# Kernel tuning notes

Hardware: AMD Instinct MI355X
Metric: run time of the kernel (lower is better)

Reference implementation:

```python
import jax, jax.numpy as jnp
import numpy as np

BATCH = 4096          # batch_size from init
TEMP = 0.1            # temperature
EPS = 1e-8            # torch CosineSimilarity eps
N = 2 * BATCH


def _neg_flat_idx(bs):
    """Static flat indices of the negative entries of the (N,N) sim matrix:
    everything except the main diagonal and the +-bs diagonals (positives)."""
    n = 2 * bs
    mask = np.ones((n, n), dtype=bool)
    np.fill_diagonal(mask, False)
    r = np.arange(bs)
    mask[r, bs + r] = False
    mask[bs + r, r] = False
    return np.nonzero(mask.reshape(-1))[0]


NEG_IDX = jnp.asarray(_neg_flat_idx(BATCH))  # (N*(N-2),)


def setup_inputs() -> dict:
    key = jax.random.key(0)
    k1, k2 = jax.random.split(key)
    msg = jax.random.normal(k1, (N, 512), dtype=jnp.float32)
    img = jax.random.normal(k2, (N, 512), dtype=jnp.float32)
    return {"msg": msg, "img": img}


def reference(msg, img):
    # cosine similarity via normalized GEMM (norms clamped at eps, per torch)
    mn = msg / jnp.maximum(jnp.linalg.norm(msg, axis=1, keepdims=True), EPS)
    im = img / jnp.maximum(jnp.linalg.norm(img, axis=1, keepdims=True), EPS)
    sim = jnp.matmul(mn, im.T) / TEMP                      # (N, N)

    sim_i_j = jnp.diagonal(sim, offset=BATCH)              # (BATCH,)
    sim_j_i = jnp.diagonal(sim, offset=-BATCH)             # (BATCH,)
    positives = jnp.concatenate([sim_i_j, sim_j_i])[:, None]   # (N, 1)
    negatives = sim.reshape(-1)[NEG_IDX].reshape(N, N - 2)     # (N, N-2)

    logits = jnp.concatenate([positives, negatives], axis=1)   # (N, N-1)
    logp = jax.nn.log_softmax(logits, axis=1)
    # labels are all zero; CrossEntropyLoss(reduction='sum') / N
    loss = -jnp.sum(logp[:, 0]) / N
    acc = jnp.mean((jnp.argmax(logits, axis=1) == 0).astype(jnp.float32))
    return loss, acc
```

## Files before the change

### kernel.cpp

```cpp
#include <hip/hip_runtime.h>
#include <hip/hip_bf16.h>


#define NROWS 8192
#define BATCHD 4096
#define DIM 512
#define BM 128
#define BN 256
#define BK 32
#define NT2 (DIM / BK)
#define SHIFT 10.0f

typedef short bf16x8 __attribute__((ext_vector_type(8)));
typedef float f32x4 __attribute__((ext_vector_type(4)));

#define GLDS(g, l)                                                             \
    __builtin_amdgcn_global_load_lds(                                          \
        (const __attribute__((address_space(1))) void*)(g),                    \
        (__attribute__((address_space(3))) void*)(l), 16, 0, 0)

__device__ __forceinline__ unsigned f2u_ord(float f) {
    unsigned u = __float_as_uint(f);
    return (u & 0x80000000u) ? ~u : (u | 0x80000000u);
}
__device__ __forceinline__ float u2f_ord(unsigned e) {
    return (e & 0x80000000u) ? __uint_as_float(e & 0x7fffffffu) : __uint_as_float(~e);
}
__device__ __forceinline__ short f2bf(float f) {
    unsigned u = __float_as_uint(f);
    return (short)((u + 0x7fffu + ((u >> 16) & 1u)) >> 16);
}

__global__ __launch_bounds__(64) void normalize_bf16_both(const float* __restrict__ msg,
                                                          const float* __restrict__ img,
                                                          short* __restrict__ mnb,
                                                          short* __restrict__ imb,
                                                          float* __restrict__ rowsum,
                                                          unsigned* __restrict__ rowmax,
                                                          float* __restrict__ accum) {
    if (blockIdx.x < 128) {
        const int i = blockIdx.x * 64 + threadIdx.x;
        rowsum[i] = 0.f;
        rowmax[i] = 0u;
        if (i < 2) accum[i] = 0.f;
    }
    int row = blockIdx.x;
    const float* in;
    short* out;
    float scale;
    if (row < NROWS) { in = msg; out = mnb; scale = 10.0f; }
    else { row -= NROWS; in = img; out = imb; scale = 1.0f; }
    const int lane = threadIdx.x;
    const float* src = in + (size_t)row * DIM + lane * 8;
    float4 v0 = *(const float4*)(src);
    float4 v1 = *(const float4*)(src + 4);
    float ss = v0.x*v0.x + v0.y*v0.y + v0.z*v0.z + v0.w*v0.w
             + v1.x*v1.x + v1.y*v1.y + v1.z*v1.z + v1.w*v1.w;
    #pragma unroll
    for (int off = 1; off < 64; off <<= 1) ss += __shfl_xor(ss, off);
    const float inv = scale / fmaxf(sqrtf(ss), 1e-8f);
    float vv[8] = {v0.x, v0.y, v0.z, v0.w, v1.x, v1.y, v1.z, v1.w};
    bf16x8 o;
    #pragma unroll
    for (int j = 0; j < 8; ++j) o[j] = f2bf(vv[j] * inv);
    *(bf16x8*)(out + (size_t)row * DIM + lane * 8) = o;
}

__global__ __launch_bounds__(512, 4) void simloss_mfma(const short* __restrict__ A,
                                                       const short* __restrict__ B,
                                                       float* __restrict__ rowsum,
                                                       unsigned* __restrict__ rowmax,
                                                       float* __restrict__ rowpos) {
    __shared__ short As[2][BM * BK];
    __shared__ short Bs[2][BN * BK];

    const int tid = threadIdx.x;
    const int lane = tid & 63;
    const int g = lane >> 4;
    const int r16 = lane & 15;
    const int wid = tid >> 6;
    const int wr = wid >> 2;
    const int wc = wid & 3;

    const int bid = blockIdx.x;
    const int xcd = bid & 7;
    const int l = bid >> 3;
    const int by = xcd * 8 + (l & 7);
    const int bx = l >> 3;
    const int rowBase = by * BM;
    const int colBase = bx * BN;

    const int srow = tid >> 2;
    const int sc = (tid & 3) ^ ((srow >> 1) & 3);
    const short* gA = A + (size_t)(rowBase + srow) * DIM + sc * 8;
    const short* gB = B + (size_t)(colBase + srow) * DIM + sc * 8;

#define STAGE(b, koff)                                      \
    do {                                                    \
        GLDS(gA + (koff), &As[b][tid * 8]);                 \
        GLDS(gB + (koff), &Bs[b][tid * 8]);                 \
        GLDS(gB + 128 * DIM + (koff), &Bs[b][4096 + tid * 8]); \
    } while (0)

    const int swz = (r16 >> 1) & 3;
    const int aBase = (wr * 64 + r16) * BK + ((g ^ swz) * 8);
    const int bBase = (wc * 64 + r16) * BK + ((g ^ swz) * 8);

    f32x4 acc[4][4] = {};

#define VMCNT(n) asm volatile("s_waitcnt vmcnt(" #n ")" ::: "memory")
#define BAR() __builtin_amdgcn_s_barrier()

    STAGE(0, 0);

    for (int t = 0; t < NT2; ++t) {
        const int b = t & 1;
        if (t < NT2 - 1) {
            STAGE(b ^ 1, (t + 1) * BK);
            VMCNT(3);
        } else {
            VMCNT(0);
        }
        BAR();
        bf16x8 af[4], bfr[4];
        #pragma unroll
        for (int m = 0; m < 4; ++m)
            af[m] = *(const bf16x8*)&As[b][aBase + m * 16 * BK];
        #pragma unroll
        for (int n = 0; n < 4; ++n)
            bfr[n] = *(const bf16x8*)&Bs[b][bBase + n * 16 * BK];
        __builtin_amdgcn_s_setprio(1);
        #pragma unroll
        for (int m = 0; m < 4; ++m)
            #pragma unroll
            for (int n = 0; n < 4; ++n)
                acc[m][n] = __builtin_amdgcn_mfma_f32_16x16x32_bf16(
                    af[m], bfr[n], acc[m][n], 0, 0, 0);
        __builtin_amdgcn_s_setprio(0);
        BAR();
    }

    __syncthreads();
    float* ssum = (float*)&As[0][0];
    float* smx = ssum + 512;
    const int baseRowW = rowBase + wr * 64 + g * 4;
    const int baseColW = colBase + wc * 64 + r16;
    #pragma unroll
    for (int m = 0; m < 4; ++m) {
        #pragma unroll
        for (int reg = 0; reg < 4; ++reg) {
            const int i = baseRowW + m * 16 + reg;
            const int partner = i ^ BATCHD;
            float sum = 0.f, mx = -1e30f;
            #pragma unroll
            for (int n = 0; n < 4; ++n) {
                const int j = baseColW + n * 16;
                const float s = acc[m][n][reg];
                const bool isDiag = (j == i);
                const bool isPos = (j == partner);
                float e = __expf(s - SHIFT);
                if (isDiag) e = 0.f;
                sum += e;
                if (!isDiag && !isPos) mx = fmaxf(mx, s);
                if (isPos) rowpos[i] = s;
            }
            #pragma unroll
            for (int off = 1; off < 16; off <<= 1) {
                sum += __shfl_xor(sum, off);
                mx = fmaxf(mx, __shfl_xor(mx, off));
            }
            if (r16 == 0) {
                const int rloc = wr * 64 + m * 16 + g * 4 + reg;
                ssum[rloc * 4 + wc] = sum;
                smx[rloc * 4 + wc] = mx;
            }
        }
    }
    __syncthreads();
    if (tid < BM) {
        const float s = ssum[tid * 4 + 0] + ssum[tid * 4 + 1] +
                        ssum[tid * 4 + 2] + ssum[tid * 4 + 3];
        const float mx = fmaxf(fmaxf(smx[tid * 4 + 0], smx[tid * 4 + 1]),
                               fmaxf(smx[tid * 4 + 2], smx[tid * 4 + 3]));
        const int i = rowBase + tid;
        atomicAdd(&rowsum[i], s);
        atomicMax(&rowmax[i], f2u_ord(mx));
    }
#undef STAGE
#undef VMCNT
#undef BAR
}

__global__ __launch_bounds__(256) void finalize_partial(const float* __restrict__ rowsum,
                                                        const unsigned* __restrict__ rowmax,
                                                        const float* __restrict__ rowpos,
                                                        float* __restrict__ accum) {
    const int tid = threadIdx.x;
    const int i = blockIdx.x * 256 + tid;
    const float lse = SHIFT + logf(rowsum[i]);
    const float pos = rowpos[i];
    float lossAcc = lse - pos;
    float hitAcc = (pos >= u2f_ord(rowmax[i])) ? 1.f : 0.f;
    __shared__ float sl[256], sa[256];
    sl[tid] = lossAcc; sa[tid] = hitAcc;
    __syncthreads();
    for (int s = 128; s > 0; s >>= 1) {
        if (tid < s) { sl[tid] += sl[tid + s]; sa[tid] += sa[tid + s]; }
        __syncthreads();
    }
    if (tid == 0) {
        atomicAdd(&accum[0], sl[0]);
        atomicAdd(&accum[1], sa[0]);
    }
}

__global__ void finalize_write(const float* __restrict__ accum, float* __restrict__ out) {
    if (threadIdx.x == 0) {
        out[0] = accum[0] / (float)NROWS;
        out[1] = accum[1] / (float)NROWS;
    }
}

extern "C" void kernel_launch(void* const* d_in, const int* in_sizes, int n_in,
                              void* d_out, int out_size, void* d_ws, size_t ws_size,
                              hipStream_t stream) {
    const float* msg = (const float*)d_in[0];
    const float* img = (const float*)d_in[1];
    float* out = (float*)d_out;

    char* ws = (char*)d_ws;
    const size_t matBytes = (size_t)NROWS * DIM * sizeof(short);
    short* mnb = (short*)ws;
    short* imb = (short*)(ws + matBytes);
    float* rowsum = (float*)(ws + 2 * matBytes);
    unsigned* rowmax = (unsigned*)(ws + 2 * matBytes + NROWS * sizeof(float));
    float* rowpos = (float*)(ws + 2 * matBytes + 2 * NROWS * sizeof(float));
    float* accum = (float*)(ws + 2 * matBytes + 3 * NROWS * sizeof(float));

    normalize_bf16_both<<<2 * NROWS, 64, 0, stream>>>(msg, img, mnb, imb,
                                                      rowsum, rowmax, accum);

    simloss_mfma<<<(NROWS / BM) * (NROWS / BN), 512, 0, stream>>>(mnb, imb, rowsum,
                                                                  rowmax, rowpos);

    finalize_partial<<<NROWS / 256, 256, 0, stream>>>(rowsum, rowmax, rowpos, accum);
    finalize_write<<<1, 64, 0, stream>>>(accum, out);
}
```

Baseline: 100.3 us.

## Switch similarity GEMM from bf16 to fp8 with 32x32x64 scaled MFMA

Normalized rows are quantized to fp8 (e4m3) instead of bf16, which halves the workspace and global/LDS traffic. The tile loop now uses BK=64 with the gfx950 scaled 32x32x64 f8f6f4 MFMA, so each wave covers its 64x64 block with 4 larger MFMAs instead of 16 smaller ones. The epilogue row/column mapping and the shuffle reductions are rewritten for the 32x32 accumulator layout. Lower precision in the logits (scaled by 10) may loosen loss and accuracy against the reference.

```diff
diff --git a/kernel.cpp b/kernel.cpp
--- a/kernel.cpp
+++ b/kernel.cpp
@@ -7,12 +7,12 @@
 #define DIM 512
 #define BM 128
 #define BN 256
-#define BK 32
-#define NT2 (DIM / BK)
+#define BK 64
+#define NSTEP (DIM / BK)
 #define SHIFT 10.0f
 
-typedef short bf16x8 __attribute__((ext_vector_type(8)));
-typedef float f32x4 __attribute__((ext_vector_type(4)));
+typedef int i32x8 __attribute__((ext_vector_type(8)));
+typedef float f32x16 __attribute__((ext_vector_type(16)));
 
 #define GLDS(g, l)                                                             \
     __builtin_amdgcn_global_load_lds(                                          \
@@ -26,18 +26,14 @@
 __device__ __forceinline__ float u2f_ord(unsigned e) {
     return (e & 0x80000000u) ? __uint_as_float(e & 0x7fffffffu) : __uint_as_float(~e);
 }
-__device__ __forceinline__ short f2bf(float f) {
-    unsigned u = __float_as_uint(f);
-    return (short)((u + 0x7fffu + ((u >> 16) & 1u)) >> 16);
-}
-
-__global__ __launch_bounds__(64) void normalize_bf16_both(const float* __restrict__ msg,
-                                                          const float* __restrict__ img,
-                                                          short* __restrict__ mnb,
-                                                          short* __restrict__ imb,
-                                                          float* __restrict__ rowsum,
-                                                          unsigned* __restrict__ rowmax,
-                                                          float* __restrict__ accum) {
+
+__global__ __launch_bounds__(64) void normalize_fp8_both(const float* __restrict__ msg,
+                                                         const float* __restrict__ img,
+                                                         unsigned char* __restrict__ mnb,
+                                                         unsigned char* __restrict__ imb,
+                                                         float* __restrict__ rowsum,
+                                                         unsigned* __restrict__ rowmax,
+                                                         float* __restrict__ accum) {
     if (blockIdx.x < 128) {
         const int i = blockIdx.x * 64 + threadIdx.x;
         rowsum[i] = 0.f;
@@ -46,7 +42,7 @@
     }
     int row = blockIdx.x;
     const float* in;
-    short* out;
+    unsigned char* out;
     float scale;
     if (row < NROWS) { in = msg; out = mnb; scale = 10.0f; }
     else { row -= NROWS; in = img; out = imb; scale = 1.0f; }
@@ -59,25 +55,25 @@
     #pragma unroll
     for (int off = 1; off < 64; off <<= 1) ss += __shfl_xor(ss, off);
     const float inv = scale / fmaxf(sqrtf(ss), 1e-8f);
-    float vv[8] = {v0.x, v0.y, v0.z, v0.w, v1.x, v1.y, v1.z, v1.w};
-    bf16x8 o;
-    #pragma unroll
-    for (int j = 0; j < 8; ++j) o[j] = f2bf(vv[j] * inv);
-    *(bf16x8*)(out + (size_t)row * DIM + lane * 8) = o;
-}
-
-__global__ __launch_bounds__(512, 4) void simloss_mfma(const short* __restrict__ A,
-                                                       const short* __restrict__ B,
+    int w0 = __builtin_amdgcn_cvt_pk_fp8_f32(v0.x * inv, v0.y * inv, 0, false);
+    w0 = __builtin_amdgcn_cvt_pk_fp8_f32(v0.z * inv, v0.w * inv, w0, true);
+    int w1 = __builtin_amdgcn_cvt_pk_fp8_f32(v1.x * inv, v1.y * inv, 0, false);
+    w1 = __builtin_amdgcn_cvt_pk_fp8_f32(v1.z * inv, v1.w * inv, w1, true);
+    *(int2*)(out + (size_t)row * DIM + lane * 8) = make_int2(w0, w1);
+}
+
+__global__ __launch_bounds__(512, 4) void simloss_mfma(const unsigned char* __restrict__ A,
+                                                       const unsigned char* __restrict__ B,
                                                        float* __restrict__ rowsum,
                                                        unsigned* __restrict__ rowmax,
                                                        float* __restrict__ rowpos) {
-    __shared__ short As[2][BM * BK];
-    __shared__ short Bs[2][BN * BK];
+    __shared__ __attribute__((aligned(16))) unsigned char As[2][BM * BK];
+    __shared__ __attribute__((aligned(16))) unsigned char Bs[2][BN * BK];
 
     const int tid = threadIdx.x;
     const int lane = tid & 63;
-    const int g = lane >> 4;
-    const int r16 = lane & 15;
+    const int r32 = lane & 31;
+    const int h = lane >> 5;
     const int wid = tid >> 6;
     const int wr = wid >> 2;
     const int wc = wid & 3;
@@ -92,50 +88,61 @@
 
     const int srow = tid >> 2;
     const int sc = (tid & 3) ^ ((srow >> 1) & 3);
-    const short* gA = A + (size_t)(rowBase + srow) * DIM + sc * 8;
-    const short* gB = B + (size_t)(colBase + srow) * DIM + sc * 8;
-
-#define STAGE(b, koff)                                      \
-    do {                                                    \
-        GLDS(gA + (koff), &As[b][tid * 8]);                 \
-        GLDS(gB + (koff), &Bs[b][tid * 8]);                 \
-        GLDS(gB + 128 * DIM + (koff), &Bs[b][4096 + tid * 8]); \
+    const unsigned char* gA = A + (size_t)(rowBase + srow) * DIM + sc * 16;
+    const unsigned char* gB = B + (size_t)(colBase + srow) * DIM + sc * 16;
+
+#define STAGE(b, koff)                                         \
+    do {                                                       \
+        GLDS(gA + (koff), &As[b][tid * 16]);                   \
+        GLDS(gB + (koff), &Bs[b][tid * 16]);                   \
+        GLDS(gB + 128 * DIM + (koff), &Bs[b][8192 + tid * 16]); \
     } while (0)
 
-    const int swz = (r16 >> 1) & 3;
-    const int aBase = (wr * 64 + r16) * BK + ((g ^ swz) * 8);
-    const int bBase = (wc * 64 + r16) * BK + ((g ^ swz) * 8);
-
-    f32x4 acc[4][4] = {};
+    const int swz = (r32 >> 1) & 3;
+    const int aAddr = (wr * 64 + r32) * BK + ((((h << 1)) ^ swz) << 4);
+    const int bAddr = (wc * 64 + r32) * BK + ((((h << 1)) ^ swz) << 4);
+
+    f32x16 acc[2][2] = {};
 
 #define VMCNT(n) asm volatile("s_waitcnt vmcnt(" #n ")" ::: "memory")
 #define BAR() __builtin_amdgcn_s_barrier()
 
     STAGE(0, 0);
 
-    for (int t = 0; t < NT2; ++t) {
+    for (int t = 0; t < NSTEP; ++t) {
         const int b = t & 1;
-        if (t < NT2 - 1) {
+        if (t < NSTEP - 1) {
             STAGE(b ^ 1, (t + 1) * BK);
             VMCNT(3);
         } else {
             VMCNT(0);
         }
         BAR();
-        bf16x8 af[4], bfr[4];
-        #pragma unroll
-        for (int m = 0; m < 4; ++m)
-            af[m] = *(const bf16x8*)&As[b][aBase + m * 16 * BK];
-        #pragma unroll
-        for (int n = 0; n < 4; ++n)
-            bfr[n] = *(const bf16x8*)&Bs[b][bBase + n * 16 * BK];
+        uint4 a0l = *(const uint4*)&As[b][aAddr];
+        uint4 a0h = *(const uint4*)&As[b][aAddr ^ 16];
+        uint4 a1l = *(const uint4*)&As[b][aAddr + 2048];
+        uint4 a1h = *(const uint4*)&As[b][(aAddr + 2048) ^ 16];
+        uint4 b0l = *(const uint4*)&Bs[b][bAddr];
+        uint4 b0h = *(const uint4*)&Bs[b][bAddr ^ 16];
+        uint4 b1l = *(const uint4*)&Bs[b][bAddr + 2048];
+        uint4 b1h = *(const uint4*)&Bs[b][(bAddr + 2048) ^ 16];
+        i32x8 af0 = {(int)a0l.x, (int)a0l.y, (int)a0l.z, (int)a0l.w,
+                     (int)a0h.x, (int)a0h.y, (int)a0h.z, (int)a0h.w};
+        i32x8 af1 = {(int)a1l.x, (int)a1l.y, (int)a1l.z, (int)a1l.w,
+                     (int)a1h.x, (int)a1h.y, (int)a1h.z, (int)a1h.w};
+        i32x8 bf0 = {(int)b0l.x, (int)b0l.y, (int)b0l.z, (int)b0l.w,
+                     (int)b0h.x, (int)b0h.y, (int)b0h.z, (int)b0h.w};
+        i32x8 bf1 = {(int)b1l.x, (int)b1l.y, (int)b1l.z, (int)b1l.w,
+                     (int)b1h.x, (int)b1h.y, (int)b1h.z, (int)b1h.w};
         __builtin_amdgcn_s_setprio(1);
-        #pragma unroll
-        for (int m = 0; m < 4; ++m)
-            #pragma unroll
-            for (int n = 0; n < 4; ++n)
-                acc[m][n] = __builtin_amdgcn_mfma_f32_16x16x32_bf16(
-                    af[m], bfr[n], acc[m][n], 0, 0, 0);
+        acc[0][0] = __builtin_amdgcn_mfma_scale_f32_32x32x64_f8f6f4(
+            af0, bf0, acc[0][0], 0, 0, 0, 0x7f7f7f7f, 0, 0x7f7f7f7f);
+        acc[0][1] = __builtin_amdgcn_mfma_scale_f32_32x32x64_f8f6f4(
+            af0, bf1, acc[0][1], 0, 0, 0, 0x7f7f7f7f, 0, 0x7f7f7f7f);
+        acc[1][0] = __builtin_amdgcn_mfma_scale_f32_32x32x64_f8f6f4(
+            af1, bf0, acc[1][0], 0, 0, 0, 0x7f7f7f7f, 0, 0x7f7f7f7f);
+        acc[1][1] = __builtin_amdgcn_mfma_scale_f32_32x32x64_f8f6f4(
+            af1, bf1, acc[1][1], 0, 0, 0, 0x7f7f7f7f, 0, 0x7f7f7f7f);
         __builtin_amdgcn_s_setprio(0);
         BAR();
     }
@@ -143,19 +150,19 @@
     __syncthreads();
     float* ssum = (float*)&As[0][0];
     float* smx = ssum + 512;
-    const int baseRowW = rowBase + wr * 64 + g * 4;
-    const int baseColW = colBase + wc * 64 + r16;
+    const int baseRow = rowBase + wr * 64 + 4 * h;
+    const int baseCol = colBase + wc * 64 + r32;
     #pragma unroll
-    for (int m = 0; m < 4; ++m) {
+    for (int ms = 0; ms < 2; ++ms) {
         #pragma unroll
-        for (int reg = 0; reg < 4; ++reg) {
-            const int i = baseRowW + m * 16 + reg;
+        for (int reg = 0; reg < 16; ++reg) {
+            const int i = baseRow + ms * 32 + (reg & 3) + 8 * (reg >> 2);
             const int partner = i ^ BATCHD;
             float sum = 0.f, mx = -1e30f;
             #pragma unroll
-            for (int n = 0; n < 4; ++n) {
-                const int j = baseColW + n * 16;
-                const float s = acc[m][n][reg];
+            for (int ns = 0; ns < 2; ++ns) {
+                const int j = baseCol + ns * 32;
+                const float s = acc[ms][ns][reg];
                 const bool isDiag = (j == i);
                 const bool isPos = (j == partner);
                 float e = __expf(s - SHIFT);
@@ -165,12 +172,12 @@
                 if (isPos) rowpos[i] = s;
             }
             #pragma unroll
-            for (int off = 1; off < 16; off <<= 1) {
+            for (int off = 1; off < 32; off <<= 1) {
                 sum += __shfl_xor(sum, off);
                 mx = fmaxf(mx, __shfl_xor(mx, off));
             }
-            if (r16 == 0) {
-                const int rloc = wr * 64 + m * 16 + g * 4 + reg;
+            if (r32 == 0) {
+                const int rloc = wr * 64 + ms * 32 + (reg & 3) + 8 * (reg >> 2) + 4 * h;
                 ssum[rloc * 4 + wc] = sum;
                 smx[rloc * 4 + wc] = mx;
             }
@@ -229,16 +236,16 @@
     float* out = (float*)d_out;
 
     char* ws = (char*)d_ws;
-    const size_t matBytes = (size_t)NROWS * DIM * sizeof(short);
-    short* mnb = (short*)ws;
-    short* imb = (short*)(ws + matBytes);
+    const size_t matBytes = (size_t)NROWS * DIM;
+    unsigned char* mnb = (unsigned char*)ws;
+    unsigned char* imb = (unsigned char*)(ws + matBytes);
     float* rowsum = (float*)(ws + 2 * matBytes);
     unsigned* rowmax = (unsigned*)(ws + 2 * matBytes + NROWS * sizeof(float));
     float* rowpos = (float*)(ws + 2 * matBytes + 2 * NROWS * sizeof(float));
     float* accum = (float*)(ws + 2 * matBytes + 3 * NROWS * sizeof(float));
 
-    normalize_bf16_both<<<2 * NROWS, 64, 0, stream>>>(msg, img, mnb, imb,
-                                                      rowsum, rowmax, accum);
+    normalize_fp8_both<<<2 * NROWS, 64, 0, stream>>>(msg, img, mnb, imb,
+                                                     rowsum, rowmax, accum);
 
     simloss_mfma<<<(NROWS / BM) * (NROWS / BN), 512, 0, stream>>>(mnb, imb, rowsum,
                                                                   rowmax, rowpos);
```

Measured after the change: 222.4 us. 122% more time.

## Enlarge GEMM tile to 256x256x64 with quarter-tile interleaved LDS staging

Applied to the files above, without the earlier changes.

Grows the fused similarity-GEMM block tile from 128x256 with K-step 32 to 256x256 with K-step 64, so each wave accumulates 8x4 MFMA tiles. The main loop now issues global-to-LDS loads for the next half-tile in interleaved quarters between MFMA groups, with an 8-way XOR swizzle. The intent is more data reuse per byte staged and better overlap of loads with MFMA work. In exchange it doubles registers and LDS per block, halving occupancy to 2 blocks per SIMD group, and adds many more barriers.

```diff
diff --git a/kernel.cpp b/kernel.cpp
--- a/kernel.cpp
+++ b/kernel.cpp
@@ -5,10 +5,9 @@
 #define NROWS 8192
 #define BATCHD 4096
 #define DIM 512
-#define BM 128
+#define BM 256
 #define BN 256
-#define BK 32
-#define NT2 (DIM / BK)
+#define BK 64
 #define SHIFT 10.0f
 
 typedef short bf16x8 __attribute__((ext_vector_type(8)));
@@ -66,7 +65,7 @@
     *(bf16x8*)(out + (size_t)row * DIM + lane * 8) = o;
 }
 
-__global__ __launch_bounds__(512, 4) void simloss_mfma(const short* __restrict__ A,
+__global__ __launch_bounds__(512, 2) void simloss_mfma(const short* __restrict__ A,
                                                        const short* __restrict__ B,
                                                        float* __restrict__ rowsum,
                                                        unsigned* __restrict__ rowmax,
@@ -78,6 +77,7 @@
     const int lane = tid & 63;
     const int g = lane >> 4;
     const int r16 = lane & 15;
+    const int swz = r16 & 7;
     const int wid = tid >> 6;
     const int wr = wid >> 2;
     const int wc = wid & 3;
@@ -85,68 +85,110 @@
     const int bid = blockIdx.x;
     const int xcd = bid & 7;
     const int l = bid >> 3;
-    const int by = xcd * 8 + (l & 7);
-    const int bx = l >> 3;
+    const int by = xcd * 4 + (l & 3);
+    const int bx = l >> 2;
     const int rowBase = by * BM;
     const int colBase = bx * BN;
 
-    const int srow = tid >> 2;
-    const int sc = (tid & 3) ^ ((srow >> 1) & 3);
-    const short* gA = A + (size_t)(rowBase + srow) * DIM + sc * 8;
-    const short* gB = B + (size_t)(colBase + srow) * DIM + sc * 8;
-
-#define STAGE(b, koff)                                      \
-    do {                                                    \
-        GLDS(gA + (koff), &As[b][tid * 8]);                 \
-        GLDS(gB + (koff), &Bs[b][tid * 8]);                 \
-        GLDS(gB + 128 * DIM + (koff), &Bs[b][4096 + tid * 8]); \
-    } while (0)
-
-    const int swz = (r16 >> 1) & 3;
-    const int aBase = (wr * 64 + r16) * BK + ((g ^ swz) * 8);
-    const int bBase = (wc * 64 + r16) * BK + ((g ^ swz) * 8);
-
-    f32x4 acc[4][4] = {};
-
+    const int rS = tid >> 3;
+    const int cS = (tid & 7) ^ (rS & 7);
+    const short* pA = A + (size_t)(rowBase + rS) * DIM + cS * 8;
+    const short* pB = B + (size_t)(colBase + rS) * DIM + cS * 8;
+
+#define STAGE_A(b, hh, koff)                                                      \
+    do {                                                                          \
+        GLDS(pA + (size_t)(hh) * 128 * DIM + (koff), &As[b][((hh)*1024 + tid) * 8]);       \
+        GLDS(pA + (size_t)((hh) * 128 + 64) * DIM + (koff), &As[b][((hh)*1024 + 512 + tid) * 8]); \
+    } while (0)
+#define STAGE_B(b, hh, koff)                                                      \
+    do {                                                                          \
+        GLDS(pB + (size_t)(hh) * 128 * DIM + (koff), &Bs[b][((hh)*1024 + tid) * 8]);       \
+        GLDS(pB + (size_t)((hh) * 128 + 64) * DIM + (koff), &Bs[b][((hh)*1024 + 512 + tid) * 8]); \
+    } while (0)
+
+    const int gk = (g ^ swz) * 8;
+    const int aRow0 = wr * 128 + r16;
+    const int bRow0 = wc * 64 + r16;
+
+    f32x4 acc[8][4] = {};
+    bf16x8 af[4][2], bf[2][2];
+
+#define LDA(b, mh)                                                             \
+    do {                                                                       \
+        _Pragma("unroll") for (int m = 0; m < 4; ++m) {                        \
+            const int ad = (aRow0 + (mh) * 64 + m * 16) * 64 + gk;             \
+            af[m][0] = *(const bf16x8*)&As[b][ad];                             \
+            af[m][1] = *(const bf16x8*)&As[b][ad ^ 32];                        \
+        }                                                                      \
+    } while (0)
+#define LDB(b, nh)                                                             \
+    do {                                                                       \
+        _Pragma("unroll") for (int n = 0; n < 2; ++n) {                        \
+            const int bd = (bRow0 + (nh) * 32 + n * 16) * 64 + gk;             \
+            bf[n][0] = *(const bf16x8*)&Bs[b][bd];                             \
+            bf[n][1] = *(const bf16x8*)&Bs[b][bd ^ 32];                        \
+        }                                                                      \
+    } while (0)
+#define MFMA16(mh, nh)                                                         \
+    do {                                                                       \
+        __builtin_amdgcn_s_setprio(1);                                         \
+        _Pragma("unroll") for (int kk = 0; kk < 2; ++kk)                       \
+            _Pragma("unroll") for (int m = 0; m < 4; ++m)                      \
+                _Pragma("unroll") for (int n = 0; n < 2; ++n)                  \
+                    acc[(mh)*4 + m][(nh)*2 + n] =                              \
+                        __builtin_amdgcn_mfma_f32_16x16x32_bf16(               \
+                            af[m][kk], bf[n][kk], acc[(mh)*4 + m][(nh)*2 + n], \
+                            0, 0, 0);                                          \
+        __builtin_amdgcn_s_setprio(0);                                         \
+    } while (0)
 #define VMCNT(n) asm volatile("s_waitcnt vmcnt(" #n ")" ::: "memory")
+#define LGKM0 asm volatile("s_waitcnt lgkmcnt(0)" ::: "memory")
 #define BAR() __builtin_amdgcn_s_barrier()
 
-    STAGE(0, 0);
-
-    for (int t = 0; t < NT2; ++t) {
-        const int b = t & 1;
-        if (t < NT2 - 1) {
-            STAGE(b ^ 1, (t + 1) * BK);
-            VMCNT(3);
-        } else {
-            VMCNT(0);
-        }
-        BAR();
-        bf16x8 af[4], bfr[4];
-        #pragma unroll
-        for (int m = 0; m < 4; ++m)
-            af[m] = *(const bf16x8*)&As[b][aBase + m * 16 * BK];
-        #pragma unroll
-        for (int n = 0; n < 4; ++n)
-            bfr[n] = *(const bf16x8*)&Bs[b][bBase + n * 16 * BK];
-        __builtin_amdgcn_s_setprio(1);
-        #pragma unroll
-        for (int m = 0; m < 4; ++m)
-            #pragma unroll
-            for (int n = 0; n < 4; ++n)
-                acc[m][n] = __builtin_amdgcn_mfma_f32_16x16x32_bf16(
-                    af[m], bfr[n], acc[m][n], 0, 0, 0);
-        __builtin_amdgcn_s_setprio(0);
-        BAR();
+    STAGE_A(0, 0, 0); STAGE_A(0, 1, 0);
+    STAGE_B(0, 0, 0); STAGE_B(0, 1, 0);
+    STAGE_A(1, 0, BK);
+    VMCNT(2);
+    BAR();
+
+    for (int j = 0; j < 4; ++j) {
+        const int k1 = (2 * j + 1) * BK;
+        const int k2 = (2 * j + 2) * BK;
+        const int k3 = (2 * j + 3) * BK;
+        const bool st = (j < 3);
+        LDA(0, 0); LDB(0, 0);
+        STAGE_A(1, 1, k1);
+        BAR(); LGKM0; MFMA16(0, 0); BAR();
+        LDB(0, 1);
+        STAGE_B(1, 0, k1);
+        BAR(); LGKM0; MFMA16(0, 1); BAR();
+        LDA(0, 1);
+        STAGE_B(1, 1, k1);
+        BAR(); LGKM0; MFMA16(1, 1); BAR();
+        LDB(0, 0);
+        if (st) { STAGE_A(0, 0, k2); VMCNT(2); } else VMCNT(0);
+        BAR(); LGKM0; MFMA16(1, 0); BAR();
+        LDA(1, 0); LDB(1, 0);
+        if (st) STAGE_A(0, 1, k2);
+        BAR(); LGKM0; MFMA16(0, 0); BAR();
+        LDB(1, 1);
+        if (st) STAGE_B(0, 0, k2);
+        BAR(); LGKM0; MFMA16(0, 1); BAR();
+        LDA(1, 1);
+        if (st) STAGE_B(0, 1, k2);
+        BAR(); LGKM0; MFMA16(1, 1); BAR();
+        LDB(1, 0);
+        if (st) { STAGE_A(1, 0, k3); VMCNT(2); }
+        BAR(); LGKM0; MFMA16(1, 0); BAR();
     }
 
     __syncthreads();
     float* ssum = (float*)&As[0][0];
-    float* smx = ssum + 512;
-    const int baseRowW = rowBase + wr * 64 + g * 4;
+    float* smx = ssum + 1024;
+    const int baseRowW = rowBase + wr * 128 + g * 4;
     const int baseColW = colBase + wc * 64 + r16;
     #pragma unroll
-    for (int m = 0; m < 4; ++m) {
+    for (int m = 0; m < 8; ++m) {
         #pragma unroll
         for (int reg = 0; reg < 4; ++reg) {
             const int i = baseRowW + m * 16 + reg;
@@ -170,14 +212,14 @@
                 mx = fmaxf(mx, __shfl_xor(mx, off));
             }
             if (r16 == 0) {
-                const int rloc = wr * 64 + m * 16 + g * 4 + reg;
+                const int rloc = wr * 128 + m * 16 + g * 4 + reg;
                 ssum[rloc * 4 + wc] = sum;
                 smx[rloc * 4 + wc] = mx;
             }
         }
     }
     __syncthreads();
-    if (tid < BM) {
+    if (tid < 256) {
         const float s = ssum[tid * 4 + 0] + ssum[tid * 4 + 1] +
                         ssum[tid * 4 + 2] + ssum[tid * 4 + 3];
         const float mx = fmaxf(fmaxf(smx[tid * 4 + 0], smx[tid * 4 + 1]),
@@ -186,8 +228,13 @@
         atomicAdd(&rowsum[i], s);
         atomicMax(&rowmax[i], f2u_ord(mx));
     }
-#undef STAGE
+#undef STAGE_A
+#undef STAGE_B
+#undef LDA
+#undef LDB
+#undef MFMA16
 #undef VMCNT
+#undef LGKM0
 #undef BAR
 }
 
```

Result: slower. 113.0 us (+12.7%).

## Switch GEMM to single-wave 64x64 blocks without barriers or LDS reduction

Applied to the files above, without the earlier changes.

Replaces the 512-thread 128x256 tile with one-wavefront blocks that each compute a 64x64 tile. This removes block barriers and the shared-memory cross-wave reduction, and each wave atomically updates the row sums and maxima directly. In exchange it reuses each staged tile less, so global/L2 traffic rises, the grid grows 8x, and global atomics increase by about 4x.

```diff
diff --git a/kernel.cpp b/kernel.cpp
--- a/kernel.cpp
+++ b/kernel.cpp
@@ -5,10 +5,9 @@
 #define NROWS 8192
 #define BATCHD 4096
 #define DIM 512
-#define BM 128
-#define BN 256
+#define BT 64
 #define BK 32
-#define NT2 (DIM / BK)
+#define NSTEP (DIM / BK)
 #define SHIFT 10.0f
 
 typedef short bf16x8 __attribute__((ext_vector_type(8)));
@@ -66,69 +65,63 @@
     *(bf16x8*)(out + (size_t)row * DIM + lane * 8) = o;
 }
 
-__global__ __launch_bounds__(512, 4) void simloss_mfma(const short* __restrict__ A,
-                                                       const short* __restrict__ B,
-                                                       float* __restrict__ rowsum,
-                                                       unsigned* __restrict__ rowmax,
-                                                       float* __restrict__ rowpos) {
-    __shared__ short As[2][BM * BK];
-    __shared__ short Bs[2][BN * BK];
+__global__ __launch_bounds__(64, 3) void simloss_mfma(const short* __restrict__ A,
+                                                      const short* __restrict__ B,
+                                                      float* __restrict__ rowsum,
+                                                      unsigned* __restrict__ rowmax,
+                                                      float* __restrict__ rowpos) {
+    __shared__ __attribute__((aligned(16))) short As[2][BT * BK];
+    __shared__ __attribute__((aligned(16))) short Bs[2][BT * BK];
 
     const int tid = threadIdx.x;
-    const int lane = tid & 63;
-    const int g = lane >> 4;
-    const int r16 = lane & 15;
-    const int wid = tid >> 6;
-    const int wr = wid >> 2;
-    const int wc = wid & 3;
+    const int g = tid >> 4;
+    const int r16 = tid & 15;
 
     const int bid = blockIdx.x;
     const int xcd = bid & 7;
     const int l = bid >> 3;
-    const int by = xcd * 8 + (l & 7);
-    const int bx = l >> 3;
-    const int rowBase = by * BM;
-    const int colBase = bx * BN;
+    const int by = xcd * 16 + (l & 15);
+    const int bx = l >> 4;
+    const int rowBase = by * BT;
+    const int colBase = bx * BT;
 
     const int srow = tid >> 2;
     const int sc = (tid & 3) ^ ((srow >> 1) & 3);
     const short* gA = A + (size_t)(rowBase + srow) * DIM + sc * 8;
     const short* gB = B + (size_t)(colBase + srow) * DIM + sc * 8;
 
-#define STAGE(b, koff)                                      \
-    do {                                                    \
-        GLDS(gA + (koff), &As[b][tid * 8]);                 \
-        GLDS(gB + (koff), &Bs[b][tid * 8]);                 \
-        GLDS(gB + 128 * DIM + (koff), &Bs[b][4096 + tid * 8]); \
+#define STAGE(b, koff)                                                  \
+    do {                                                                \
+        _Pragma("unroll") for (int i = 0; i < 4; ++i) {                 \
+            GLDS(gA + (size_t)i * 16 * DIM + (koff), &As[b][i * 512 + tid * 8]); \
+            GLDS(gB + (size_t)i * 16 * DIM + (koff), &Bs[b][i * 512 + tid * 8]); \
+        }                                                               \
     } while (0)
 
     const int swz = (r16 >> 1) & 3;
-    const int aBase = (wr * 64 + r16) * BK + ((g ^ swz) * 8);
-    const int bBase = (wc * 64 + r16) * BK + ((g ^ swz) * 8);
+    const int aBase = r16 * BK + ((g ^ swz) * 8);
 
     f32x4 acc[4][4] = {};
 
 #define VMCNT(n) asm volatile("s_waitcnt vmcnt(" #n ")" ::: "memory")
-#define BAR() __builtin_amdgcn_s_barrier()
 
     STAGE(0, 0);
 
-    for (int t = 0; t < NT2; ++t) {
+    for (int t = 0; t < NSTEP; ++t) {
         const int b = t & 1;
-        if (t < NT2 - 1) {
+        if (t < NSTEP - 1) {
             STAGE(b ^ 1, (t + 1) * BK);
-            VMCNT(3);
+            VMCNT(8);
         } else {
             VMCNT(0);
         }
-        BAR();
         bf16x8 af[4], bfr[4];
         #pragma unroll
         for (int m = 0; m < 4; ++m)
             af[m] = *(const bf16x8*)&As[b][aBase + m * 16 * BK];
         #pragma unroll
         for (int n = 0; n < 4; ++n)
-            bfr[n] = *(const bf16x8*)&Bs[b][bBase + n * 16 * BK];
+            bfr[n] = *(const bf16x8*)&Bs[b][aBase + n * 16 * BK];
         __builtin_amdgcn_s_setprio(1);
         #pragma unroll
         for (int m = 0; m < 4; ++m)
@@ -137,24 +130,20 @@
                 acc[m][n] = __builtin_amdgcn_mfma_f32_16x16x32_bf16(
                     af[m], bfr[n], acc[m][n], 0, 0, 0);
         __builtin_amdgcn_s_setprio(0);
-        BAR();
-    }
-
-    __syncthreads();
-    float* ssum = (float*)&As[0][0];
-    float* smx = ssum + 512;
-    const int baseRowW = rowBase + wr * 64 + g * 4;
-    const int baseColW = colBase + wc * 64 + r16;
+    }
+
+    const int baseRow = rowBase + g * 4;
+    const int baseCol = colBase + r16;
     #pragma unroll
     for (int m = 0; m < 4; ++m) {
         #pragma unroll
         for (int reg = 0; reg < 4; ++reg) {
-            const int i = baseRowW + m * 16 + reg;
+            const int i = baseRow + m * 16 + reg;
             const int partner = i ^ BATCHD;
             float sum = 0.f, mx = -1e30f;
             #pragma unroll
             for (int n = 0; n < 4; ++n) {
-                const int j = baseColW + n * 16;
+                const int j = baseCol + n * 16;
                 const float s = acc[m][n][reg];
                 const bool isDiag = (j == i);
                 const bool isPos = (j == partner);
@@ -170,25 +159,13 @@
                 mx = fmaxf(mx, __shfl_xor(mx, off));
             }
             if (r16 == 0) {
-                const int rloc = wr * 64 + m * 16 + g * 4 + reg;
-                ssum[rloc * 4 + wc] = sum;
-                smx[rloc * 4 + wc] = mx;
+                atomicAdd(&rowsum[i], sum);
+                atomicMax(&rowmax[i], f2u_ord(mx));
             }
         }
     }
-    __syncthreads();
-    if (tid < BM) {
-        const float s = ssum[tid * 4 + 0] + ssum[tid * 4 + 1] +
-                        ssum[tid * 4 + 2] + ssum[tid * 4 + 3];
-        const float mx = fmaxf(fmaxf(smx[tid * 4 + 0], smx[tid * 4 + 1]),
-                               fmaxf(smx[tid * 4 + 2], smx[tid * 4 + 3]));
-        const int i = rowBase + tid;
-        atomicAdd(&rowsum[i], s);
-        atomicMax(&rowmax[i], f2u_ord(mx));
-    }
 #undef STAGE
 #undef VMCNT
-#undef BAR
 }
 
 __global__ __launch_bounds__(256) void finalize_partial(const float* __restrict__ rowsum,
@@ -240,8 +217,8 @@
     normalize_bf16_both<<<2 * NROWS, 64, 0, stream>>>(msg, img, mnb, imb,
                                                       rowsum, rowmax, accum);
 
-    simloss_mfma<<<(NROWS / BM) * (NROWS / BN), 512, 0, stream>>>(mnb, imb, rowsum,
-                                                                  rowmax, rowpos);
+    simloss_mfma<<<(NROWS / BT) * (NROWS / BT), 64, 0, stream>>>(mnb, imb, rowsum,
+                                                                 rowmax, rowpos);
 
     finalize_partial<<<NROWS / 256, 256, 0, stream>>>(rowsum, rowmax, rowpos, accum);
     finalize_write<<<1, 64, 0, stream>>>(accum, out);
```

Result: slower. 171.6 us (+71.1%).
